# Kernel tuning notes

Measured on AMD Instinct MI355X. Metric: run time of the kernel, lower is better.

The kernel has to match this reference:

```python
import jax, jax.numpy as jnp
import numpy as np

BATCH = 16384
IN_F = 768
OUT_F = 768
GRID_SIZE = 8           # act_fun.get_size()
GRID_LO, GRID_HI = -2.0, 2.0


def rbf_basis(x):
    """Gaussian RBF spline basis: [b, i] -> [b, a, i]."""
    grid = jnp.linspace(GRID_LO, GRID_HI, GRID_SIZE, dtype=x.dtype)  # [a]
    h = (GRID_HI - GRID_LO) / (GRID_SIZE - 1)
    z = (x[:, None, :] - grid[None, :, None]) / h                    # [b, a, i]
    return jnp.exp(-z * z)


def setup_inputs() -> dict:
    key = jax.random.key(0)
    k1, k2, k3 = jax.random.split(key, 3)
    x = jax.random.normal(k1, (BATCH, IN_F), dtype=jnp.float32)
    # xavier_normal_(gain=0.001): std = 0.001 * sqrt(2 / (fan_in + fan_out))
    std_wb = 0.001 * np.sqrt(2.0 / (IN_F + OUT_F))
    w_b = jax.random.normal(k2, (OUT_F, IN_F), dtype=jnp.float32) * std_wb
    w_s = jnp.ones((OUT_F, IN_F), dtype=jnp.float32)
    c = jax.random.normal(k3, (GRID_SIZE, OUT_F, IN_F), dtype=jnp.float32) * 0.001
    return {"x": x, "w_b": w_b, "w_s": w_s, "c": c}


def reference(x, w_b, w_s, c):
    # Original: sum_i[ (sum_a phi(x)_{bai} c_{aoi}) * w_s_{oi} + silu(x)_{bi} * w_b_{oi} ]
    phi = rbf_basis(x)                       # [b, a, i]
    cw = c * w_s[None, :, :]                 # fold scale into coeffs: [a, o, i]
    spline = jnp.einsum('bai,aoi->bo', phi, cw)   # fused contraction over (a, i)
    res = jax.nn.silu(x) @ w_b.T             # [b, o]
    return spline + res
```

## Files before the change

### kernel.cpp

```cpp
#include <hip/hip_runtime.h>
#include <hip/hip_bf16.h>

#define BATCH 16384
#define INF 768
#define OUTF 768
#define NSLAB 9
#define KTOT (NSLAB * INF)
#define BM 128
#define BN 128
#define BK 64
#define KB_TILES 12
#define NTILES (NSLAB * KB_TILES)

#define LOG2E 1.4426950408889634f
#define EXPM2 0.13533528323661270f

#define TILE_SH 8192
#define IB_SH   8192
#define SLAB_SH (KB_TILES * TILE_SH)

typedef __bf16 bf16x8 __attribute__((ext_vector_type(8)));
typedef float f32x4 __attribute__((ext_vector_type(4)));
typedef unsigned short ushort8v __attribute__((ext_vector_type(8)));

__device__ __forceinline__ unsigned short f2bf(float f) {
  unsigned u = __builtin_bit_cast(unsigned, f);
  u += 0x7fffu + ((u >> 16) & 1u);
  return (unsigned short)(u >> 16);
}

__device__ __forceinline__ unsigned cvt2(float a, float b) {
  unsigned r;
  asm("v_cvt_pk_bf16_f32 %0, %1, %2" : "=v"(r) : "v"(a), "v"(b));
  return r;
}

__device__ __forceinline__ bf16x8 pack8(const f32x4 a, const f32x4 b) {
  union { uint4 u; bf16x8 v; } r;
  r.u.x = cvt2(a[0], a[1]); r.u.y = cvt2(a[2], a[3]);
  r.u.z = cvt2(b[0], b[1]); r.u.w = cvt2(b[2], b[3]);
  return r.v;
}

__device__ __forceinline__ void gload_lds16(const void* g, void* l) {
  __builtin_amdgcn_global_load_lds(
      (const __attribute__((address_space(1))) unsigned int*)g,
      (__attribute__((address_space(3))) unsigned int*)l, 16, 0, 0);
}

__global__ __launch_bounds__(256) void build_bext2(
    const float* __restrict__ w_b, const float* __restrict__ w_s,
    const float* __restrict__ c, unsigned short* __restrict__ bt) {
  const int gid = blockIdx.x * 256 + threadIdx.x;
  const int lane = gid & 63;
  const int q = (gid >> 6) & 3;
  const int wv = (gid >> 8) & 3;
  const int tile = gid >> 10;
  const int kt = tile % NTILES;
  const int cbq = tile / NTILES;
  const int a = kt / KB_TILES;
  const int ib = kt - a * KB_TILES;
  const int rg = lane >> 3, chh = lane & 7;
  const int o = cbq * 128 + wv * 32 + q * 8 + rg;
  const int i = ib * 64 + (chh ^ rg) * 8;

  float4 v0, v1;
  if (a < 8) {
    const float* cp = c + ((size_t)(a * OUTF + o)) * INF + i;
    const float* wp = w_s + (size_t)o * INF + i;
    const float4 c0 = *(const float4*)cp, c1 = *(const float4*)(cp + 4);
    const float4 s0 = *(const float4*)wp, s1 = *(const float4*)(wp + 4);
    v0 = make_float4(c0.x * s0.x, c0.y * s0.y, c0.z * s0.z, c0.w * s0.w);
    v1 = make_float4(c1.x * s1.x, c1.y * s1.y, c1.z * s1.z, c1.w * s1.w);
  } else {
    const float* bp = w_b + (size_t)o * INF + i;
    v0 = *(const float4*)bp;
    v1 = *(const float4*)(bp + 4);
  }
  ushort8v r;
  r[0] = f2bf(v0.x); r[1] = f2bf(v0.y); r[2] = f2bf(v0.z); r[3] = f2bf(v0.w);
  r[4] = f2bf(v1.x); r[5] = f2bf(v1.y); r[6] = f2bf(v1.z); r[7] = f2bf(v1.w);
  *(ushort8v*)(bt + (size_t)gid * 8) = r;
}

__global__ __launch_bounds__(256, 2) void kan_gemm9(
    const float* __restrict__ x, const unsigned short* __restrict__ bt,
    float* __restrict__ out) {
  __shared__ unsigned short Bs[3][BN * BK];

  const int orig = blockIdx.x;
  const int bid = (orig & 7) * 96 + (orig >> 3);
  const int cb = bid / (BATCH / BM);
  const int rb = bid - cb * (BATCH / BM);
  const int row0 = rb * BM, col0 = cb * BN;

  const int t = threadIdx.x;
  const int lane = t & 63;
  const int w = t >> 6;
  const int lrow = lane & 15, lhi = lane >> 4;

  f32x4 acc[2][8];
#pragma unroll
  for (int mt = 0; mt < 2; ++mt)
#pragma unroll
    for (int n = 0; n < 8; ++n)
      acc[mt][n] = (f32x4){0.f, 0.f, 0.f, 0.f};

  const unsigned short* gt =
      bt + (size_t)cb * NTILES * TILE_SH + w * 2048 + lane * 8;
  const float* xb = x + (size_t)(row0 + w * 32 + lrow) * INF;

  const int c0 = lhi ^ (lrow & 7);
  const int c1 = (4 + lhi) ^ (lrow & 7);
  const unsigned short* pB0 = &Bs[0][lrow * 64 + c0 * 8];
  const unsigned short* pB1 = &Bs[0][lrow * 64 + c1 * 8];

  f32x4 ph[2][2][2], gg[2][2][2];
  bf16x8 afc[2][2];

  auto stage = [&](const unsigned short* src, int slot) {
#pragma unroll
    for (int q = 0; q < 4; ++q)
      gload_lds16(src + q * 512, &Bs[slot][w * 2048 + q * 512]);
  };

  auto mma_kk = [&](int kk, int slot) {
    const unsigned short* pB = kk ? pB1 : pB0;
#pragma unroll
    for (int n = 0; n < 8; ++n) {
      const bf16x8 b = *(const bf16x8*)(pB + slot * TILE_SH + n * 1024);
      acc[0][n] = __builtin_amdgcn_mfma_f32_16x16x32_bf16(afc[kk][0], b, acc[0][n], 0, 0, 0);
      acc[1][n] = __builtin_amdgcn_mfma_f32_16x16x32_bf16(afc[kk][1], b, acc[1][n], 0, 0, 0);
    }
  };

  f32x4 xr[2][2][2];
  auto load_x = [&](int ib) {
#pragma unroll
    for (int mt = 0; mt < 2; ++mt)
#pragma unroll
      for (int kk = 0; kk < 2; ++kk) {
        const float* p = xb + ib * BK + mt * 16 * INF + kk * 32 + lhi * 8;
        xr[mt][kk][0] = *(const f32x4*)p;
        xr[mt][kk][1] = *(const f32x4*)(p + 4);
      }
  };
  auto silu_init = [&]() {
#pragma unroll
    for (int kk = 0; kk < 2; ++kk)
#pragma unroll
      for (int mt = 0; mt < 2; ++mt) {
        const f32x4 x0 = xr[mt][kk][0], x1 = xr[mt][kk][1];
        f32x4 s0, s1;
#pragma unroll
        for (int e = 0; e < 4; ++e) {
          s0[e] = x0[e] * __builtin_amdgcn_rcpf(
                      1.f + __builtin_amdgcn_exp2f(x0[e] * (-LOG2E)));
          s1[e] = x1[e] * __builtin_amdgcn_rcpf(
                      1.f + __builtin_amdgcn_exp2f(x1[e] * (-LOG2E)));
        }
        afc[kk][mt] = pack8(s0, s1);
        const f32x4 z0 = x0 * 1.75f + 3.5f;
        const f32x4 z1 = x1 * 1.75f + 3.5f;
#pragma unroll
        for (int e = 0; e < 4; ++e) {
          ph[mt][kk][0][e] = __builtin_amdgcn_exp2f(-(z0[e] * z0[e]) * LOG2E);
          ph[mt][kk][1][e] = __builtin_amdgcn_exp2f(-(z1[e] * z1[e]) * LOG2E);
          gg[mt][kk][0][e] = __builtin_amdgcn_exp2f(z0[e] * (2.f * LOG2E) - LOG2E);
          gg[mt][kk][1][e] = __builtin_amdgcn_exp2f(z1[e] * (2.f * LOG2E) - LOG2E);
        }
      }
  };
  auto pack_advance = [&]() {
#pragma unroll
    for (int kk = 0; kk < 2; ++kk)
#pragma unroll
      for (int mt = 0; mt < 2; ++mt) {
        afc[kk][mt] = pack8(ph[mt][kk][0], ph[mt][kk][1]);
        ph[mt][kk][0] *= gg[mt][kk][0];
        ph[mt][kk][1] *= gg[mt][kk][1];
        gg[mt][kk][0] = gg[mt][kk][0] * EXPM2;
        gg[mt][kk][1] = gg[mt][kk][1] * EXPM2;
      }
  };

  load_x(0);
  const unsigned short* gib = gt;
  stage(gib + 8 * SLAB_SH, 0);
  stage(gib, 1);
  silu_init();
  asm volatile("s_waitcnt vmcnt(4)" ::: "memory");
  __builtin_amdgcn_s_barrier();
  __builtin_amdgcn_sched_barrier(0);

#pragma clang loop unroll(disable)
  for (int ib = 0; ib < KB_TILES; ++ib) {
    const bool last = (ib == KB_TILES - 1);
#pragma unroll
    for (int j = 0; j < 9; ++j) {
      const int slot = j % 3;

      if (j == 8 && !last) load_x(ib + 1);

      if (j <= 6) {
        stage(gib + (j + 1) * SLAB_SH, (j + 2) % 3);
      } else if (!last) {
        if (j == 7) stage(gib + 8 * SLAB_SH + IB_SH, 0);
        else        stage(gib + IB_SH, 1);
      }

      mma_kk(0, slot);
      mma_kk(1, slot);

      if (j < 8)       pack_advance();
      else if (!last)  silu_init();

      if (!last || j < 7) {
        asm volatile("s_waitcnt vmcnt(4)" ::: "memory");
      } else if (j == 7) {
        asm volatile("s_waitcnt vmcnt(0)" ::: "memory");
      }
      if (!(last && j == 8)) {
        __builtin_amdgcn_s_barrier();
        __builtin_amdgcn_sched_barrier(0);
      }
    }
    gib += IB_SH;
  }

#pragma unroll
  for (int mt = 0; mt < 2; ++mt) {
#pragma unroll
    for (int n = 0; n < 8; ++n) {
      const int row = row0 + w * 32 + mt * 16 + lhi * 4;
      const int col = col0 + n * 16 + lrow;
#pragma unroll
      for (int r = 0; r < 4; ++r)
        out[(size_t)(row + r) * OUTF + col] = acc[mt][n][r];
    }
  }
}

__device__ __forceinline__ float phi_f(float x, float g) {
  float z = (x - g) * 1.75f;
  return __expf(-z * z);
}
__device__ __forceinline__ float silu_f(float x) {
  return x / (1.f + __expf(-x));
}

__global__ __launch_bounds__(256, 2) void kan_gemm_fb(
    const float* __restrict__ x, const float* __restrict__ w_b,
    const float* __restrict__ w_s, const float* __restrict__ c,
    float* __restrict__ out) {
  __shared__ unsigned short As[128][72];
  __shared__ unsigned short Bs[128][72];

  const int bid = blockIdx.x;
  const int cbf = bid % (OUTF / 128);
  const int rbf = bid / (OUTF / 128);
  const int row0 = rbf * 128, col0 = cbf * 128;

  const int t = threadIdx.x;
  const int lane = t & 63;
  const int w = t >> 6;
  const int wr = w >> 1, wc = w & 1;
  const int lrow = lane & 15, lhi = lane >> 4;

  f32x4 acc[4][4];
#pragma unroll
  for (int m = 0; m < 4; ++m)
#pragma unroll
    for (int n = 0; n < 4; ++n)
      acc[m][n] = (f32x4){0.f, 0.f, 0.f, 0.f};

  const int rsub = t >> 4;
  const int k4 = t & 15;

  for (int kt = 0; kt < KTOT / 64; ++kt) {
    const int a = kt / (INF / 64);
    const int i0 = (kt % (INF / 64)) * 64;
    const float ga = -2.f + (float)a * (4.f / 7.f);

#pragma unroll
    for (int p = 0; p < 8; ++p) {
      const int r = p * 16 + rsub;
      const float4 xv = *(const float4*)(x + (size_t)(row0 + r) * INF + i0 + k4 * 4);
      ushort4 av;
      if (a < 8) {
        av.x = f2bf(phi_f(xv.x, ga)); av.y = f2bf(phi_f(xv.y, ga));
        av.z = f2bf(phi_f(xv.z, ga)); av.w = f2bf(phi_f(xv.w, ga));
      } else {
        av.x = f2bf(silu_f(xv.x)); av.y = f2bf(silu_f(xv.y));
        av.z = f2bf(silu_f(xv.z)); av.w = f2bf(silu_f(xv.w));
      }
      *(ushort4*)&As[r][k4 * 4] = av;

      ushort4 bv;
      if (a < 8) {
        const float4 cv = *(const float4*)(c + ((size_t)a * OUTF + col0 + r) * INF + i0 + k4 * 4);
        const float4 wv = *(const float4*)(w_s + (size_t)(col0 + r) * INF + i0 + k4 * 4);
        bv.x = f2bf(cv.x * wv.x); bv.y = f2bf(cv.y * wv.y);
        bv.z = f2bf(cv.z * wv.z); bv.w = f2bf(cv.w * wv.w);
      } else {
        const float4 bbv = *(const float4*)(w_b + (size_t)(col0 + r) * INF + i0 + k4 * 4);
        bv.x = f2bf(bbv.x); bv.y = f2bf(bbv.y);
        bv.z = f2bf(bbv.z); bv.w = f2bf(bbv.w);
      }
      *(ushort4*)&Bs[r][k4 * 4] = bv;
    }
    __syncthreads();

#pragma unroll
    for (int kk = 0; kk < 2; ++kk) {
      bf16x8 af[4], bfr[4];
#pragma unroll
      for (int m = 0; m < 4; ++m)
        af[m] = *(const bf16x8*)&As[wr * 64 + m * 16 + lrow][kk * 32 + lhi * 8];
#pragma unroll
      for (int n = 0; n < 4; ++n)
        bfr[n] = *(const bf16x8*)&Bs[wc * 64 + n * 16 + lrow][kk * 32 + lhi * 8];
#pragma unroll
      for (int m = 0; m < 4; ++m)
#pragma unroll
        for (int n = 0; n < 4; ++n)
          acc[m][n] = __builtin_amdgcn_mfma_f32_16x16x32_bf16(af[m], bfr[n], acc[m][n], 0, 0, 0);
    }
    __syncthreads();
  }

#pragma unroll
  for (int m = 0; m < 4; ++m) {
#pragma unroll
    for (int n = 0; n < 4; ++n) {
      const int row = row0 + wr * 64 + m * 16 + lhi * 4;
      const int col = col0 + wc * 64 + n * 16 + lrow;
#pragma unroll
      for (int r = 0; r < 4; ++r)
        out[(size_t)(row + r) * OUTF + col] = acc[m][n][r];
    }
  }
}

extern "C" void kernel_launch(void* const* d_in, const int* in_sizes, int n_in,
                              void* d_out, int out_size, void* d_ws, size_t ws_size,
                              hipStream_t stream) {
  const float* x   = (const float*)d_in[0];
  const float* w_b = (const float*)d_in[1];
  const float* w_s = (const float*)d_in[2];
  const float* c   = (const float*)d_in[3];
  float* out = (float*)d_out;

  const size_t need = (size_t)OUTF * KTOT * sizeof(unsigned short);
  if (ws_size >= need) {
    unsigned short* bt = (unsigned short*)d_ws;
    build_bext2<<<(OUTF * KTOT / 8) / 256, 256, 0, stream>>>(w_b, w_s, c, bt);
    kan_gemm9<<<(BATCH / BM) * (OUTF / BN), 256, 0, stream>>>(x, bt, out);
  } else {
    kan_gemm_fb<<<(BATCH / 128) * (OUTF / 128), 256, 0, stream>>>(x, w_b, w_s, c, out);
  }
}
```

Baseline: 202.0 us.

## Widen GEMM output tile to 192 columns to reuse RBF A-fragments more

Raises the N tile width from 128 to 192, so each block covers 128x192 outputs and the grid shrinks from 768 to 512 blocks. The B-matrix prebuild kernel is reorganised for the new tile layout, and the staging loop and wait counts are adjusted to six async loads per tile. Each block's computed RBF/SiLU A-fragments and x reads are now reused across more output columns, cutting the per-output exp and pack work. In exchange the accumulator and register footprint grow, LDS per stage grows, and 512 blocks may fill the GPU's compute units less evenly.

```diff
diff --git a/kernel.cpp b/kernel.cpp
--- a/kernel.cpp
+++ b/kernel.cpp
@@ -7,17 +7,20 @@
 #define NSLAB 9
 #define KTOT (NSLAB * INF)
 #define BM 128
-#define BN 128
+#define BN 192
 #define BK 64
 #define KB_TILES 12
 #define NTILES (NSLAB * KB_TILES)
+#define NRB (BATCH / BM)
+#define NCB (OUTF / BN)
 
 #define LOG2E 1.4426950408889634f
 #define EXPM2 0.13533528323661270f
 
-#define TILE_SH 8192
-#define IB_SH   8192
+#define TILE_SH (BN * BK)
+#define IB_SH   TILE_SH
 #define SLAB_SH (KB_TILES * TILE_SH)
+#define CB_SH   ((size_t)NTILES * TILE_SH)
 
 typedef __bf16 bf16x8 __attribute__((ext_vector_type(8)));
 typedef float f32x4 __attribute__((ext_vector_type(4)));
@@ -48,21 +51,22 @@
       (__attribute__((address_space(3))) unsigned int*)l, 16, 0, 0);
 }
 
-__global__ __launch_bounds__(256) void build_bext2(
+__global__ __launch_bounds__(256) void build_bext3(
     const float* __restrict__ w_b, const float* __restrict__ w_s,
     const float* __restrict__ c, unsigned short* __restrict__ bt) {
   const int gid = blockIdx.x * 256 + threadIdx.x;
-  const int lane = gid & 63;
-  const int q = (gid >> 6) & 3;
-  const int wv = (gid >> 8) & 3;
-  const int tile = gid >> 10;
-  const int kt = tile % NTILES;
+  const int tile = gid / 1536;
+  const int g = gid - tile * 1536;
+  const int q = g >> 8;
+  const int tt = g & 255;
+  const int row = q * 32 + (tt >> 3);
+  const int ch = tt & 7;
   const int cbq = tile / NTILES;
+  const int kt = tile - cbq * NTILES;
   const int a = kt / KB_TILES;
   const int ib = kt - a * KB_TILES;
-  const int rg = lane >> 3, chh = lane & 7;
-  const int o = cbq * 128 + wv * 32 + q * 8 + rg;
-  const int i = ib * 64 + (chh ^ rg) * 8;
+  const int o = cbq * BN + row;
+  const int i = ib * 64 + (ch ^ (row & 7)) * 8;
 
   float4 v0, v1;
   if (a < 8) {
@@ -83,15 +87,15 @@
   *(ushort8v*)(bt + (size_t)gid * 8) = r;
 }
 
-__global__ __launch_bounds__(256, 2) void kan_gemm9(
+__global__ __launch_bounds__(256, 2) void kan_gemm10(
     const float* __restrict__ x, const unsigned short* __restrict__ bt,
     float* __restrict__ out) {
-  __shared__ unsigned short Bs[3][BN * BK];
+  __shared__ unsigned short Bs[3][TILE_SH];
 
   const int orig = blockIdx.x;
-  const int bid = (orig & 7) * 96 + (orig >> 3);
-  const int cb = bid / (BATCH / BM);
-  const int rb = bid - cb * (BATCH / BM);
+  const int bid = (orig & 7) * 64 + (orig >> 3);
+  const int cb = bid / NRB;
+  const int rb = bid - cb * NRB;
   const int row0 = rb * BM, col0 = cb * BN;
 
   const int t = threadIdx.x;
@@ -99,15 +103,14 @@
   const int w = t >> 6;
   const int lrow = lane & 15, lhi = lane >> 4;
 
-  f32x4 acc[2][8];
+  f32x4 acc[2][12];
 #pragma unroll
   for (int mt = 0; mt < 2; ++mt)
 #pragma unroll
-    for (int n = 0; n < 8; ++n)
+    for (int n = 0; n < 12; ++n)
       acc[mt][n] = (f32x4){0.f, 0.f, 0.f, 0.f};
 
-  const unsigned short* gt =
-      bt + (size_t)cb * NTILES * TILE_SH + w * 2048 + lane * 8;
+  const unsigned short* gt = bt + (size_t)cb * CB_SH + t * 8;
   const float* xb = x + (size_t)(row0 + w * 32 + lrow) * INF;
 
   const int c0 = lhi ^ (lrow & 7);
@@ -120,14 +123,14 @@
 
   auto stage = [&](const unsigned short* src, int slot) {
 #pragma unroll
-    for (int q = 0; q < 4; ++q)
-      gload_lds16(src + q * 512, &Bs[slot][w * 2048 + q * 512]);
+    for (int q = 0; q < 6; ++q)
+      gload_lds16(src + q * 2048, &Bs[slot][q * 2048 + t * 8]);
   };
 
   auto mma_kk = [&](int kk, int slot) {
     const unsigned short* pB = kk ? pB1 : pB0;
 #pragma unroll
-    for (int n = 0; n < 8; ++n) {
+    for (int n = 0; n < 12; ++n) {
       const bf16x8 b = *(const bf16x8*)(pB + slot * TILE_SH + n * 1024);
       acc[0][n] = __builtin_amdgcn_mfma_f32_16x16x32_bf16(afc[kk][0], b, acc[0][n], 0, 0, 0);
       acc[1][n] = __builtin_amdgcn_mfma_f32_16x16x32_bf16(afc[kk][1], b, acc[1][n], 0, 0, 0);
@@ -189,7 +192,7 @@
   stage(gib + 8 * SLAB_SH, 0);
   stage(gib, 1);
   silu_init();
-  asm volatile("s_waitcnt vmcnt(4)" ::: "memory");
+  asm volatile("s_waitcnt vmcnt(6)" ::: "memory");
   __builtin_amdgcn_s_barrier();
   __builtin_amdgcn_sched_barrier(0);
 
@@ -216,7 +219,7 @@
       else if (!last)  silu_init();
 
       if (!last || j < 7) {
-        asm volatile("s_waitcnt vmcnt(4)" ::: "memory");
+        asm volatile("s_waitcnt vmcnt(6)" ::: "memory");
       } else if (j == 7) {
         asm volatile("s_waitcnt vmcnt(0)" ::: "memory");
       }
@@ -231,7 +234,7 @@
 #pragma unroll
   for (int mt = 0; mt < 2; ++mt) {
 #pragma unroll
-    for (int n = 0; n < 8; ++n) {
+    for (int n = 0; n < 12; ++n) {
       const int row = row0 + w * 32 + mt * 16 + lhi * 4;
       const int col = col0 + n * 16 + lrow;
 #pragma unroll
@@ -354,8 +357,8 @@
   const size_t need = (size_t)OUTF * KTOT * sizeof(unsigned short);
   if (ws_size >= need) {
     unsigned short* bt = (unsigned short*)d_ws;
-    build_bext2<<<(OUTF * KTOT / 8) / 256, 256, 0, stream>>>(w_b, w_s, c, bt);
-    kan_gemm9<<<(BATCH / BM) * (OUTF / BN), 256, 0, stream>>>(x, bt, out);
+    build_bext3<<<(NCB * NTILES * 1536) / 256, 256, 0, stream>>>(w_b, w_s, c, bt);
+    kan_gemm10<<<NRB * NCB, 256, 0, stream>>>(x, bt, out);
   } else {
     kan_gemm_fb<<<(BATCH / 128) * (OUTF / 128), 256, 0, stream>>>(x, w_b, w_s, c, out);
   }
```

Result: slower. 277.2 us (+37.3%).
